# Kernel tuning notes

Hardware: AMD Instinct MI355X
Metric: run time of the kernel (lower is better)

## Reference

```python
import jax, jax.numpy as jnp
import numpy as np

V = 200000  # num entities
R = 100     # num relations
D = 128     # embedding_dim
K = 20      # entity_neighbor_num
B = 128     # batch (docs)
N = 50      # entities per doc


def setup_inputs() -> dict:
    key = jax.random.key(0)
    ks = jax.random.split(key, 8)
    return {
        "entity_ids": jax.random.randint(ks[0], (B, N), 0, V),
        "adj_entity": jax.random.randint(ks[1], (V, K), 0, V),
        "adj_relation": jax.random.randint(ks[2], (V, K), 0, R),
        "entity_embedding": jax.random.normal(ks[3], (V, D), jnp.float32),
        "relation_embedding": jax.random.normal(ks[4], (R, D), jnp.float32),
        "W_att": jax.random.normal(ks[5], (3 * D, 1), jnp.float32) * 0.05,
        "b_att": jnp.zeros((1,), jnp.float32),
        "W_conv": jax.random.normal(ks[6], (2 * D, D), jnp.float32) * 0.05,
        "b_conv": jnp.zeros((D,), jnp.float32),
    }


def reference(entity_ids, adj_entity, adj_relation, entity_embedding,
              relation_embedding, W_att, b_att, W_conv, b_conv):
    # neighbor ids: [B, N, K]
    neigh_ent = adj_entity[entity_ids]
    neigh_rel = adj_relation[entity_ids]
    ne = entity_embedding[neigh_ent]      # [B, N, K, D]
    nr = relation_embedding[neigh_rel]    # [B, N, K, D]
    ee = entity_embedding[entity_ids]     # [B, N, D]
    ee_exp = jnp.broadcast_to(ee[:, :, None, :], ne.shape)  # [B, N, K, D]
    concat = jnp.concatenate([ee_exp, ne, nr], axis=-1)     # [B, N, K, 3D]
    logits = jax.nn.relu(concat @ W_att + b_att)            # [B, N, K, 1]
    # NOTE: faithful to original nn.Softmax(dim=0) -> softmax over batch axis
    att = jax.nn.softmax(logits, axis=0)                    # [B, N, K, 1]
    neighbor_att = jnp.sum(att * ne, axis=2)                # [B, N, D]
    agg_in = jnp.concatenate([ee, neighbor_att], axis=-1)   # [B, N, 2D]
    return jax.nn.relu(agg_in @ W_conv + b_conv)            # [B, N, D]
```

## Files before the change

### kernel.cpp

```cpp
#include <hip/hip_runtime.h>

#define V 200000
#define R 100
#define D 128
#define K 20
#define B 128
#define N 50

__global__ void k_logits(const int* __restrict__ eids,
                         const int* __restrict__ adjE,
                         const int* __restrict__ adjR,
                         const float* __restrict__ EE,
                         const float* __restrict__ RE,
                         const float* __restrict__ Watt,
                         const float* __restrict__ batt,
                         float* __restrict__ att) {
  const int lane = threadIdx.x & 63;
  const int wv   = threadIdx.x >> 6;
  const int bn   = blockIdx.x * 4 + wv;
  const int b = bn / N;
  const int n = bn % N;
  const int eid = eids[bn];

  const float2 wa_e = ((const float2*)Watt)[lane];
  const float2 e2   = ((const float2*)(EE + (size_t)eid * D))[lane];
  float p = e2.x * wa_e.x + e2.y * wa_e.y;
  #pragma unroll
  for (int off = 32; off > 0; off >>= 1) p += __shfl_down(p, off);
  const float s_ee = __shfl(p, 0) + batt[0];

  const int g  = lane >> 4;
  const int sl = lane & 15;
  const float4* wnp = (const float4*)(Watt + D + 8 * sl);
  const float4* wrp = (const float4*)(Watt + 2 * D + 8 * sl);
  const float4 wn0 = wnp[0], wn1 = wnp[1];
  const float4 wr0 = wrp[0], wr1 = wrp[1];

  const int* ae = adjE + eid * K;
  const int* ar = adjR + eid * K;

  float q[5];
  #pragma unroll
  for (int k5 = 0; k5 < 5; ++k5) {
    const int k = k5 * 4 + g;
    const int nid = ae[k];
    const int rid = ar[k];
    const float4* np = (const float4*)(EE + (size_t)nid * D + 8 * sl);
    const float4* rp = (const float4*)(RE + (size_t)rid * D + 8 * sl);
    const float4 n0 = np[0], n1 = np[1];
    const float4 r0 = rp[0], r1 = rp[1];
    float s = n0.x * wn0.x + n0.y * wn0.y + n0.z * wn0.z + n0.w * wn0.w
            + n1.x * wn1.x + n1.y * wn1.y + n1.z * wn1.z + n1.w * wn1.w
            + r0.x * wr0.x + r0.y * wr0.y + r0.z * wr0.z + r0.w * wr0.w
            + r1.x * wr1.x + r1.y * wr1.y + r1.z * wr1.z + r1.w * wr1.w;
    #pragma unroll
    for (int off = 8; off > 0; off >>= 1) s += __shfl_down(s, off, 16);
    q[k5] = s;
  }

  if (sl == 0) {
    #pragma unroll
    for (int k5 = 0; k5 < 5; ++k5) {
      const int k = k5 * 4 + g;
      const float logit = s_ee + q[k5];
      att[(n * K + k) * B + b] = logit > 0.0f ? logit : 0.0f;
    }
  }
}

__global__ void k_softmax(float* __restrict__ att) {
  __shared__ float red[4];
  const int gg = blockIdx.x;
  const int t = threadIdx.x;
  const float x = att[gg * B + t];

  float m = x;
  #pragma unroll
  for (int off = 32; off > 0; off >>= 1) m = fmaxf(m, __shfl_down(m, off));
  if ((t & 63) == 0) red[t >> 6] = m;
  __syncthreads();
  const float mm = fmaxf(red[0], red[1]);

  const float e = __expf(x - mm);
  float s = e;
  #pragma unroll
  for (int off = 32; off > 0; off >>= 1) s += __shfl_down(s, off);
  if ((t & 63) == 0) red[2 + (t >> 6)] = s;
  __syncthreads();
  const float ss = red[2] + red[3];

  att[gg * B + t] = e / ss;
}

#define G 8
__global__ void k_out(const int* __restrict__ eids,
                      const int* __restrict__ adjE,
                      const float* __restrict__ EE,
                      const float* __restrict__ att,
                      const float* __restrict__ Wc,
                      const float* __restrict__ bc,
                      float* __restrict__ out) {
  __shared__ float agg[G][2 * D];
  __shared__ float part[2][G][D];
  __shared__ float s_att[G][K];
  __shared__ int   s_nid[G][K];

  const int t = threadIdx.x;
  const int d = t & 127;
  const int h = t >> 7;
  const int base = blockIdx.x * G;

  if (t < G * K) {
    const int j = t / K, k = t % K;
    const int bn = base + j;
    const int b = bn / N;
    const int n = bn % N;
    const int eid = eids[bn];
    s_nid[j][k] = adjE[eid * K + k];
    s_att[j][k] = att[(n * K + k) * B + b];
  }
  __syncthreads();

  #pragma unroll
  for (int jj = 0; jj < G / 2; ++jj) {
    const int j = h + jj * 2;
    const int bn = base + j;
    const int eid = eids[bn];
    const float ee = EE[(size_t)eid * D + d];
    float na = 0.0f;
    #pragma unroll
    for (int k = 0; k < K; ++k)
      na += s_att[j][k] * EE[(size_t)s_nid[j][k] * D + d];
    agg[j][d] = ee;
    agg[j][D + d] = na;
  }
  __syncthreads();

  float acc[G];
  #pragma unroll
  for (int j = 0; j < G; ++j) acc[j] = 0.0f;
  const int ibase = h * D;
  for (int c = 0; c < 32; ++c) {
    const int i = ibase + c * 4;
    const float w0 = Wc[(i + 0) * D + d];
    const float w1 = Wc[(i + 1) * D + d];
    const float w2 = Wc[(i + 2) * D + d];
    const float w3 = Wc[(i + 3) * D + d];
    #pragma unroll
    for (int j = 0; j < G; ++j) {
      const float4 a = *(const float4*)&agg[j][i];
      acc[j] += a.x * w0 + a.y * w1 + a.z * w2 + a.w * w3;
    }
  }
  #pragma unroll
  for (int j = 0; j < G; ++j) part[h][j][d] = acc[j];
  __syncthreads();

  const float bb = bc[d];
  #pragma unroll
  for (int jj = 0; jj < G / 2; ++jj) {
    const int j = h + jj * 2;
    const float v = part[0][j][d] + part[1][j][d] + bb;
    out[(size_t)(base + j) * D + d] = v > 0.0f ? v : 0.0f;
  }
}

extern "C" void kernel_launch(void* const* d_in, const int* in_sizes, int n_in,
                              void* d_out, int out_size, void* d_ws, size_t ws_size,
                              hipStream_t stream) {
  const int*   eids = (const int*)d_in[0];
  const int*   adjE = (const int*)d_in[1];
  const int*   adjR = (const int*)d_in[2];
  const float* EE   = (const float*)d_in[3];
  const float* RE   = (const float*)d_in[4];
  const float* Watt = (const float*)d_in[5];
  const float* batt = (const float*)d_in[6];
  const float* Wc   = (const float*)d_in[7];
  const float* bc   = (const float*)d_in[8];
  float* out = (float*)d_out;

  float* att = (float*)d_ws;

  k_logits<<<(B * N) / 4, 256, 0, stream>>>(eids, adjE, adjR, EE, RE, Watt,
                                            batt, att);
  k_softmax<<<N * K, 128, 0, stream>>>(att);
  k_out<<<(B * N) / G, 256, 0, stream>>>(eids, adjE, EE, att, Wc, bc, out);
}
```

Measured before the change: 207.8 us.

## Fold exp into logits kernel, compute only inverse sums, widen k_out group

```diff
diff --git a/kernel.cpp b/kernel.cpp
--- a/kernel.cpp
+++ b/kernel.cpp
@@ -14,7 +14,7 @@
                          const float* __restrict__ RE,
                          const float* __restrict__ Watt,
                          const float* __restrict__ batt,
-                         float* __restrict__ att) {
+                         float* __restrict__ att_e) {
   const int lane = threadIdx.x & 63;
   const int wv   = threadIdx.x >> 6;
   const int bn   = blockIdx.x * 4 + wv;
@@ -63,40 +63,29 @@
     for (int k5 = 0; k5 < 5; ++k5) {
       const int k = k5 * 4 + g;
       const float logit = s_ee + q[k5];
-      att[(n * K + k) * B + b] = logit > 0.0f ? logit : 0.0f;
+      const float rl = logit > 0.0f ? logit : 0.0f;
+      att_e[(n * K + k) * B + b] = __expf(rl);
     }
   }
 }
 
-__global__ void k_softmax(float* __restrict__ att) {
-  __shared__ float red[4];
-  const int gg = blockIdx.x;
-  const int t = threadIdx.x;
-  const float x = att[gg * B + t];
-
-  float m = x;
-  #pragma unroll
-  for (int off = 32; off > 0; off >>= 1) m = fmaxf(m, __shfl_down(m, off));
-  if ((t & 63) == 0) red[t >> 6] = m;
-  __syncthreads();
-  const float mm = fmaxf(red[0], red[1]);
-
-  const float e = __expf(x - mm);
-  float s = e;
+__global__ void k_sum(const float* __restrict__ att_e,
+                      float* __restrict__ inv_sum) {
+  const int g    = blockIdx.x * 4 + (threadIdx.x >> 6);
+  const int lane = threadIdx.x & 63;
+  const float2 e2 = ((const float2*)(att_e + g * B))[lane];
+  float s = e2.x + e2.y;
   #pragma unroll
   for (int off = 32; off > 0; off >>= 1) s += __shfl_down(s, off);
-  if ((t & 63) == 0) red[2 + (t >> 6)] = s;
-  __syncthreads();
-  const float ss = red[2] + red[3];
-
-  att[gg * B + t] = e / ss;
+  if (lane == 0) inv_sum[g] = 1.0f / s;
 }
 
-#define G 8
+#define G 16
 __global__ void k_out(const int* __restrict__ eids,
                       const int* __restrict__ adjE,
                       const float* __restrict__ EE,
-                      const float* __restrict__ att,
+                      const float* __restrict__ att_e,
+                      const float* __restrict__ inv_sum,
                       const float* __restrict__ Wc,
                       const float* __restrict__ bc,
                       float* __restrict__ out) {
@@ -110,14 +99,15 @@
   const int h = t >> 7;
   const int base = blockIdx.x * G;
 
-  if (t < G * K) {
-    const int j = t / K, k = t % K;
+  for (int s = t; s < G * K; s += 256) {
+    const int j = s / K, k = s % K;
     const int bn = base + j;
     const int b = bn / N;
     const int n = bn % N;
     const int eid = eids[bn];
+    const int g = n * K + k;
     s_nid[j][k] = adjE[eid * K + k];
-    s_att[j][k] = att[(n * K + k) * B + b];
+    s_att[j][k] = att_e[g * B + b] * inv_sum[g];
   }
   __syncthreads();
 
@@ -179,10 +169,12 @@
   const float* bc   = (const float*)d_in[8];
   float* out = (float*)d_out;
 
-  float* att = (float*)d_ws;
+  float* att_e   = (float*)d_ws;
+  float* inv_sum = att_e + (size_t)N * K * B;
 
   k_logits<<<(B * N) / 4, 256, 0, stream>>>(eids, adjE, adjR, EE, RE, Watt,
-                                            batt, att);
-  k_softmax<<<N * K, 128, 0, stream>>>(att);
-  k_out<<<(B * N) / G, 256, 0, stream>>>(eids, adjE, EE, att, Wc, bc, out);
+                                            batt, att_e);
+  k_sum<<<(N * K) / 4, 256, 0, stream>>>(att_e, inv_sum);
+  k_out<<<(B * N) / G, 256, 0, stream>>>(eids, adjE, EE, att_e, inv_sum,
+                                         Wc, bc, out);
 }
```

Measured after the change: 208.9 us. Within noise of the previous version (+0.5%).
